# Kernel tuning notes

Hardware: AMD Instinct MI355X
Metric: run time of the kernel (lower is better)

The kernel has to match this reference:

```python
import jax, jax.numpy as jnp
import numpy as np
from jax import lax


def _conv(x, w, b, padding):
    # x: NCHW, w: OIHW
    y = lax.conv_general_dilated(x, w, (1, 1), padding,
                                 dimension_numbers=('NCHW', 'OIHW', 'NCHW'))
    return y + b[None, :, None, None]


def setup_inputs() -> dict:
    key = jax.random.key(0)
    ks = jax.random.split(key, 24)
    B = 64
    d = {
        'p2': jax.random.normal(ks[0], (B, 128, 64, 128), jnp.float32),
        'p3': jax.random.normal(ks[1], (B, 128, 32, 64), jnp.float32),
        'p4': jax.random.normal(ks[2], (B, 128, 16, 32), jnp.float32),
        'p5': jax.random.normal(ks[3], (B, 512, 8, 16), jnp.float32),
    }
    def w(k, shape, fan_in):
        return jax.random.normal(k, shape, jnp.float32) * (1.0 / np.sqrt(fan_in))
    # smooth convs 3x3, 128->128
    for i, name in enumerate(['s1', 's2', 's3']):
        d['w_' + name] = w(ks[4 + 2 * i], (128, 128, 3, 3), 128 * 9)
        d['b_' + name] = jnp.zeros((128,), jnp.float32)
    # tidy convs 1x1
    tidy_cin = [128, 128, 128, 512]
    for i in range(4):
        d['w_t%d' % (i + 1)] = w(ks[10 + i], (1, tidy_cin[i], 1, 1), tidy_cin[i])
        d['b_t%d' % (i + 1)] = jnp.zeros((1,), jnp.float32)
    # pl convs (kH,1) on single channel
    pl_kh = [64, 32, 16, 8]
    for i in range(4):
        d['w_pl%d' % (i + 1)] = w(ks[14 + i], (1, 1, pl_kh[i], 1), pl_kh[i])
        d['b_pl%d' % (i + 1)] = jnp.zeros((1,), jnp.float32)
    return d


def reference(p2, p3, p4, p5,
              w_s1, b_s1, w_s2, b_s2, w_s3, b_s3,
              w_t1, b_t1, w_t2, b_t2, w_t3, b_t3, w_t4, b_t4,
              w_pl1, b_pl1, w_pl2, b_pl2, w_pl3, b_pl3, w_pl4, b_pl4):
    B = p2.shape[0]
    # smooth + relu (p5 has no smooth in the original module)
    q2 = jax.nn.relu(_conv(p2, w_s1, b_s1, 'SAME'))
    q3 = jax.nn.relu(_conv(p3, w_s2, b_s2, 'SAME'))
    q4 = jax.nn.relu(_conv(p4, w_s3, b_s3, 'SAME'))
    # tidy 1x1 -> single score channel
    t1 = _conv(q2, w_t1, b_t1, 'VALID')
    t2 = _conv(q3, w_t2, b_t2, 'VALID')
    t3 = _conv(q4, w_t3, b_t3, 'VALID')
    t4 = _conv(p5, w_t4, b_t4, 'VALID')
    # column-pooling convs collapse height to 1 -> per-column scores
    c1 = _conv(t1, w_pl1, b_pl1, 'VALID').reshape(B, -1)  # [B,128]
    c2 = _conv(t2, w_pl2, b_pl2, 'VALID').reshape(B, -1)  # [B,64]
    c3 = _conv(t3, w_pl3, b_pl3, 'VALID').reshape(B, -1)  # [B,32]
    c4 = _conv(t4, w_pl4, b_pl4, 'VALID').reshape(B, -1)  # [B,16]
    return jnp.concatenate([c1, c2, c3, c4], axis=1)      # [B,240]
```

## Files before the change

### kernel.cpp

```cpp
#include <hip/hip_runtime.h>


typedef short s8v __attribute__((ext_vector_type(8)));
typedef float f4v __attribute__((ext_vector_type(4)));

__device__ __forceinline__ unsigned short f32_bf16_rne(float f) {
  union { float f; unsigned int u; } v;
  v.f = f;
  unsigned int u = v.u;
  u += 0x7FFFu + ((u >> 16) & 1u);
  return (unsigned short)(u >> 16);
}

__global__ void prep_w_k(const float* __restrict__ w1,
                         const float* __restrict__ w2,
                         const float* __restrict__ w3,
                         unsigned short* __restrict__ out) {
  int idx = blockIdx.x * 256 + threadIdx.x;
  if (idx >= 442368) return;
  int i    = idx & 7;
  int cout = (idx >> 3) & 127;
  int t    = idx >> 10;
  int qg = t & 3; t >>= 2;
  int kw = t % 3; t /= 3;
  int kh = t % 3; t /= 3;
  int chunk = t & 3; t >>= 2;
  int s = t;
  const float* w = (s == 0) ? w1 : ((s == 1) ? w2 : w3);
  int cin = chunk * 32 + qg * 8 + i;
  out[idx] = f32_bf16_rne(w[((cout * 128 + cin) * 3 + kh) * 3 + kw]);
}

__global__ void init_out_k(float* __restrict__ out,
                           const float* bt1, const float* bt2,
                           const float* bt3, const float* bt4,
                           const float* wpl1, const float* bpl1,
                           const float* wpl2, const float* bpl2,
                           const float* wpl3, const float* bpl3,
                           const float* wpl4, const float* bpl4) {
  int idx = blockIdx.x * 256 + threadIdx.x;
  if (idx >= 64 * 240) return;
  int c = idx % 240;
  const float* wpl; const float* bpl; const float* bt; int H;
  if (c < 128)      { wpl = wpl1; bpl = bpl1; bt = bt1; H = 64; }
  else if (c < 192) { wpl = wpl2; bpl = bpl2; bt = bt2; H = 32; }
  else if (c < 224) { wpl = wpl3; bpl = bpl3; bt = bt3; H = 16; }
  else              { wpl = wpl4; bpl = bpl4; bt = bt4; H = 8;  }
  float s = 0.f;
  for (int h = 0; h < H; ++h) s += wpl[h];
  out[idx] = bt[0] * s + bpl[0];
}

__global__ void level4_k(const float* __restrict__ p5,
                         const float* __restrict__ w_t4,
                         const float* __restrict__ w_pl4,
                         float* __restrict__ out) {
  int b = blockIdx.x;
  int z = blockIdx.y;
  int t = threadIdx.x;
  int w = t & 15, g = t >> 4;
  const float* base = p5 + (size_t)b * 65536 + z * 16384;
  const float* wt = w_t4 + z * 128;
  float acc = 0.f;
  for (int j = g; j < 1024; j += 16) {
    acc += wt[j >> 3] * w_pl4[j & 7] * base[j * 16 + w];
  }
  acc += __shfl_xor(acc, 16);
  acc += __shfl_xor(acc, 32);
  if ((t & 48) == 0) atomicAdd(&out[b * 240 + 224 + w], acc);
}

template<int H, int W, int R, int COLBASE>
__global__ __launch_bounds__(256, 2)
void conv_level_k(const float* __restrict__ p,
                  const unsigned short* __restrict__ wl,
                  const float* __restrict__ b_s,
                  const float* __restrict__ w_t,
                  const float* __restrict__ w_pl,
                  float* __restrict__ out) {
  constexpr int ROWS = R + 2;
  constexpr int WP = W + 2;
  constexpr int HW = H * W;
  constexpr int NIT = 4 * ROWS * WP;
  __shared__ __align__(16) unsigned short Xs[4][ROWS][WP][8];
  __shared__ __align__(16) unsigned short Ws[3][4][128][8];

  const int tid = threadIdx.x;
  const int wave = tid >> 6, lane = tid & 63;
  const int lm = lane & 15, q = lane >> 4;
  const int h0 = blockIdx.x * R;
  const int b  = blockIdx.y;

  int rr[4], ww[4], xbase[4];
#pragma unroll
  for (int nt = 0; nt < 4; ++nt) {
    int n = wave * 64 + nt * 16 + lm;
    rr[nt] = n / W;
    ww[nt] = n % W;
    xbase[nt] = ((q * ROWS + rr[nt]) * WP + ww[nt]) * 16;
  }
  const int woff = (q * 128 + lm) * 16;

  f4v acc[8][4];
#pragma unroll
  for (int mt = 0; mt < 8; ++mt)
#pragma unroll
    for (int nt = 0; nt < 4; ++nt)
      acc[mt][nt] = (f4v){0.f, 0.f, 0.f, 0.f};

  const s8v Z8 = {0, 0, 0, 0, 0, 0, 0, 0};
  const float* pb = p + (size_t)b * 128 * HW;
  const char* XsB = (const char*)&Xs[0][0][0][0];
  const char* WsB = (const char*)&Ws[0][0][0][0];

  s8v wreg[6];
  const unsigned short* wseg = wl + wave * 512 + lane * 8;
  unsigned short* wdst = &Ws[0][0][0][0] + wave * 512 + lane * 8;

#define LOAD_W(chunk, kh) do {                                        \
    const unsigned short* _s = wseg + ((chunk) * 3 + (kh)) * 12288;   \
    _Pragma("unroll")                                                 \
    for (int s = 0; s < 6; ++s) wreg[s] = *(const s8v*)(_s + s * 2048); \
  } while (0)

#define STORE_W() do {                                                \
    _Pragma("unroll")                                                 \
    for (int s = 0; s < 6; ++s) *(s8v*)(wdst + s * 2048) = wreg[s];   \
  } while (0)

  LOAD_W(0, 0);

  for (int chunk = 0; chunk < 4; ++chunk) {
    __syncthreads();
    for (int it = tid; it < NIT; it += 256) {
      int pos = it % WP;
      int rem = it / WP;
      int row = rem % ROWS;
      int qg  = rem / ROWS;
      int h_in = h0 + row - 1;
      int w_g  = pos - 1;
      s8v v = Z8;
      if (h_in >= 0 && h_in < H && w_g >= 0 && w_g < W) {
        const float* src = pb + (size_t)(chunk * 32 + qg * 8) * HW + h_in * W + w_g;
#pragma unroll
        for (int i = 0; i < 8; ++i) v[i] = (short)f32_bf16_rne(src[(size_t)i * HW]);
      }
      *(s8v*)&Xs[qg][row][pos][0] = v;
    }
    STORE_W();
    __syncthreads();

#pragma unroll
    for (int kh = 0; kh < 3; ++kh) {
      int nc = (kh == 2) ? ((chunk < 3) ? chunk + 1 : 3) : chunk;
      int nk = (kh == 2) ? 0 : kh + 1;
      LOAD_W(nc, nk);

      int xk[4];
#pragma unroll
      for (int nt = 0; nt < 4; ++nt) xk[nt] = xbase[nt] + kh * (WP * 16);

#pragma unroll
      for (int kw = 0; kw < 3; ++kw) {
        s8v bf[4];
#pragma unroll
        for (int nt = 0; nt < 4; ++nt)
          bf[nt] = *(const s8v*)(XsB + xk[nt] + kw * 16);
#pragma unroll
        for (int mt = 0; mt < 8; ++mt) {
          s8v af = *(const s8v*)(WsB + kw * 8192 + mt * 256 + woff);
#pragma unroll
          for (int nt = 0; nt < 4; ++nt)
            acc[mt][nt] = __builtin_amdgcn_mfma_f32_16x16x32_bf16(af, bf[nt], acc[mt][nt], 0, 0, 0);
        }
      }
      if (kh < 2) {
        __syncthreads();
        STORE_W();
        __syncthreads();
      }
    }
  }
#undef LOAD_W
#undef STORE_W

#pragma unroll
  for (int nt = 0; nt < 4; ++nt) {
    float s = 0.f;
#pragma unroll
    for (int mt = 0; mt < 8; ++mt) {
#pragma unroll
      for (int rg = 0; rg < 4; ++rg) {
        int cout = mt * 16 + q * 4 + rg;
        float v = fmaxf(acc[mt][nt][rg] + b_s[cout], 0.f);
        s = fmaf(w_t[cout], v, s);
      }
    }
    s *= w_pl[h0 + rr[nt]];
    s += __shfl_xor(s, 16);
    s += __shfl_xor(s, 32);
    if (lane < 16) atomicAdd(&out[b * 240 + COLBASE + ww[nt]], s);
  }
}

extern "C" void kernel_launch(void* const* d_in, const int* in_sizes, int n_in,
                              void* d_out, int out_size, void* d_ws, size_t ws_size,
                              hipStream_t stream) {
  (void)in_sizes; (void)n_in; (void)out_size; (void)ws_size;
  const float* p2   = (const float*)d_in[0];
  const float* p3   = (const float*)d_in[1];
  const float* p4   = (const float*)d_in[2];
  const float* p5   = (const float*)d_in[3];
  const float* w_s1 = (const float*)d_in[4];
  const float* b_s1 = (const float*)d_in[5];
  const float* w_s2 = (const float*)d_in[6];
  const float* b_s2 = (const float*)d_in[7];
  const float* w_s3 = (const float*)d_in[8];
  const float* b_s3 = (const float*)d_in[9];
  const float* w_t1 = (const float*)d_in[10];
  const float* b_t1 = (const float*)d_in[11];
  const float* w_t2 = (const float*)d_in[12];
  const float* b_t2 = (const float*)d_in[13];
  const float* w_t3 = (const float*)d_in[14];
  const float* b_t3 = (const float*)d_in[15];
  const float* w_t4 = (const float*)d_in[16];
  const float* b_t4 = (const float*)d_in[17];
  const float* w_pl1 = (const float*)d_in[18];
  const float* b_pl1 = (const float*)d_in[19];
  const float* w_pl2 = (const float*)d_in[20];
  const float* b_pl2 = (const float*)d_in[21];
  const float* w_pl3 = (const float*)d_in[22];
  const float* b_pl3 = (const float*)d_in[23];
  const float* w_pl4 = (const float*)d_in[24];
  const float* b_pl4 = (const float*)d_in[25];

  unsigned short* wp = (unsigned short*)d_ws;
  float* out = (float*)d_out;

  prep_w_k<<<dim3(1728), dim3(256), 0, stream>>>(w_s1, w_s2, w_s3, wp);
  init_out_k<<<dim3(60), dim3(256), 0, stream>>>(out, b_t1, b_t2, b_t3, b_t4,
                                                 w_pl1, b_pl1, w_pl2, b_pl2,
                                                 w_pl3, b_pl3, w_pl4, b_pl4);
  conv_level_k<64, 128, 2, 0><<<dim3(32, 64), dim3(256), 0, stream>>>(
      p2, wp, b_s1, w_t1, w_pl1, out);
  conv_level_k<32, 64, 4, 128><<<dim3(8, 64), dim3(256), 0, stream>>>(
      p3, wp + 147456, b_s2, w_t2, w_pl2, out);
  conv_level_k<16, 32, 8, 192><<<dim3(2, 64), dim3(256), 0, stream>>>(
      p4, wp + 294912, b_s3, w_t3, w_pl3, out);
  level4_k<<<dim3(64, 4), dim3(256), 0, stream>>>(p5, w_t4, w_pl4, out);
}
```

Before: 680.1 us.

## Restructure conv kernel to one output row per block with double-buffered pipelined loads

```diff
diff --git a/kernel.cpp b/kernel.cpp
--- a/kernel.cpp
+++ b/kernel.cpp
@@ -3,6 +3,8 @@
 
 typedef short s8v __attribute__((ext_vector_type(8)));
 typedef float f4v __attribute__((ext_vector_type(4)));
+
+#define BARRIER() asm volatile("s_waitcnt lgkmcnt(0)\n\ts_barrier" ::: "memory")
 
 __device__ __forceinline__ unsigned short f32_bf16_rne(float f) {
   union { float f; unsigned int u; } v;
@@ -70,136 +72,168 @@
   if ((t & 48) == 0) atomicAdd(&out[b * 240 + 224 + w], acc);
 }
 
-template<int H, int W, int R, int COLBASE>
+template<int H, int W, int COLBASE>
 __global__ __launch_bounds__(256, 2)
-void conv_level_k(const float* __restrict__ p,
+void conv_fused_k(const float* __restrict__ p,
                   const unsigned short* __restrict__ wl,
                   const float* __restrict__ b_s,
                   const float* __restrict__ w_t,
                   const float* __restrict__ w_pl,
                   float* __restrict__ out) {
-  constexpr int ROWS = R + 2;
   constexpr int WP = W + 2;
+  constexpr int NT = (W >= 128) ? 2 : 1;
+  constexpr int AW = W / (16 * NT);
   constexpr int HW = H * W;
-  constexpr int NIT = 4 * ROWS * WP;
-  __shared__ __align__(16) unsigned short Xs[4][ROWS][WP][8];
-  __shared__ __align__(16) unsigned short Ws[3][4][128][8];
+  constexpr int SLOTS = 4 * W;
+  constexpr int SPT = (SLOTS + 255) / 256;
+  __shared__ __align__(16) unsigned short Xs[4][3][WP][8];
+  __shared__ __align__(16) unsigned short Ws[2][3][4][128][8];
 
   const int tid = threadIdx.x;
   const int wave = tid >> 6, lane = tid & 63;
   const int lm = lane & 15, q = lane >> 4;
-  const int h0 = blockIdx.x * R;
+  const int h0 = blockIdx.x;
   const int b  = blockIdx.y;
-
-  int rr[4], ww[4], xbase[4];
-#pragma unroll
-  for (int nt = 0; nt < 4; ++nt) {
-    int n = wave * 64 + nt * 16 + lm;
-    rr[nt] = n / W;
-    ww[nt] = n % W;
-    xbase[nt] = ((q * ROWS + rr[nt]) * WP + ww[nt]) * 16;
-  }
-  const int woff = (q * 128 + lm) * 16;
-
-  f4v acc[8][4];
-#pragma unroll
-  for (int mt = 0; mt < 8; ++mt)
-#pragma unroll
-    for (int nt = 0; nt < 4; ++nt)
-      acc[mt][nt] = (f4v){0.f, 0.f, 0.f, 0.f};
-
-  const s8v Z8 = {0, 0, 0, 0, 0, 0, 0, 0};
   const float* pb = p + (size_t)b * 128 * HW;
-  const char* XsB = (const char*)&Xs[0][0][0][0];
-  const char* WsB = (const char*)&Ws[0][0][0][0];
-
+
+  int sqg[SPT], swp[SPT];
+  bool sok[SPT];
+  const float* sbase[SPT];
+#pragma unroll
+  for (int k = 0; k < SPT; ++k) {
+    int slot = tid + 256 * k;
+    sok[k] = (SLOTS % 256 == 0) ? true : (slot < SLOTS);
+    int qg = slot / W;
+    int wp_ = slot % W;
+    sqg[k] = qg; swp[k] = wp_;
+    sbase[k] = pb + (size_t)(qg * 8) * HW + wp_;
+  }
+  bool rok[3]; int hin[3];
+#pragma unroll
+  for (int r = 0; r < 3; ++r) { hin[r] = h0 + r - 1; rok[r] = (hin[r] >= 0) && (hin[r] < H); }
+
+  float xf[SPT][8];
   s8v wreg[6];
   const unsigned short* wseg = wl + wave * 512 + lane * 8;
-  unsigned short* wdst = &Ws[0][0][0][0] + wave * 512 + lane * 8;
-
-#define LOAD_W(chunk, kh) do {                                        \
-    const unsigned short* _s = wseg + ((chunk) * 3 + (kh)) * 12288;   \
-    _Pragma("unroll")                                                 \
-    for (int s = 0; s < 6; ++s) wreg[s] = *(const s8v*)(_s + s * 2048); \
-  } while (0)
-
-#define STORE_W() do {                                                \
-    _Pragma("unroll")                                                 \
-    for (int s = 0; s < 6; ++s) *(s8v*)(wdst + s * 2048) = wreg[s];   \
-  } while (0)
-
-  LOAD_W(0, 0);
-
-  for (int chunk = 0; chunk < 4; ++chunk) {
-    __syncthreads();
-    for (int it = tid; it < NIT; it += 256) {
-      int pos = it % WP;
-      int rem = it / WP;
-      int row = rem % ROWS;
-      int qg  = rem / ROWS;
-      int h_in = h0 + row - 1;
-      int w_g  = pos - 1;
-      s8v v = Z8;
-      if (h_in >= 0 && h_in < H && w_g >= 0 && w_g < W) {
-        const float* src = pb + (size_t)(chunk * 32 + qg * 8) * HW + h_in * W + w_g;
-#pragma unroll
-        for (int i = 0; i < 8; ++i) v[i] = (short)f32_bf16_rne(src[(size_t)i * HW]);
-      }
-      *(s8v*)&Xs[qg][row][pos][0] = v;
-    }
-    STORE_W();
-    __syncthreads();
-
+  unsigned short* wdstbase = &Ws[0][0][0][0][0] + wave * 512 + lane * 8;
+
+  auto issueW = [&](int t) {
+    const unsigned short* s = wseg + t * 12288;
+#pragma unroll
+    for (int j = 0; j < 6; ++j) wreg[j] = *(const s8v*)(s + j * 2048);
+  };
+  auto writeW = [&](int buf) {
+    unsigned short* d = wdstbase + buf * 12288;
+#pragma unroll
+    for (int j = 0; j < 6; ++j) *(s8v*)(d + j * 2048) = wreg[j];
+  };
+  auto issueXa = [&](float (*arr)[8], int c, int r) {
+#pragma unroll
+    for (int k = 0; k < SPT; ++k) {
+      if (sok[k] && rok[r]) {
+        const float* s = sbase[k] + (size_t)(c * 32) * HW + (size_t)hin[r] * W;
+#pragma unroll
+        for (int i = 0; i < 8; ++i) arr[k][i] = s[(size_t)i * HW];
+      } else {
+#pragma unroll
+        for (int i = 0; i < 8; ++i) arr[k][i] = 0.f;
+      }
+    }
+  };
+  auto writeXa = [&](float (*arr)[8], int r) {
+#pragma unroll
+    for (int k = 0; k < SPT; ++k) {
+      if (sok[k]) {
+        s8v v;
+#pragma unroll
+        for (int i = 0; i < 8; ++i) v[i] = (short)f32_bf16_rne(arr[k][i]);
+        *(s8v*)&Xs[sqg[k]][r][1 + swp[k]][0] = v;
+      }
+    }
+  };
+
+  if (tid < 24) {
+    int qg = tid / 6, r2 = tid % 6;
+    const s8v Z = {0, 0, 0, 0, 0, 0, 0, 0};
+    *(s8v*)&Xs[qg][r2 >> 1][(r2 & 1) ? (WP - 1) : 0][0] = Z;
+  }
+  {
+    float xr0[SPT][8], xr1[SPT][8];
+    issueW(0);
+    issueXa(xr0, 0, 0);
+    issueXa(xr1, 0, 1);
+    issueXa(xf, 0, 2);
+    writeW(0);
+    issueW(1);
+    writeXa(xr0, 0);
+    writeXa(xr1, 1);
+  }
+  BARRIER();
+
+  f4v acc[8][NT];
+#pragma unroll
+  for (int mt = 0; mt < 8; ++mt)
+#pragma unroll
+    for (int t = 0; t < NT; ++t)
+      acc[mt][t] = (f4v){0.f, 0.f, 0.f, 0.f};
+
+  for (int c = 0; c < 4; ++c) {
 #pragma unroll
     for (int kh = 0; kh < 3; ++kh) {
-      int nc = (kh == 2) ? ((chunk < 3) ? chunk + 1 : 3) : chunk;
-      int nk = (kh == 2) ? 0 : kh + 1;
-      LOAD_W(nc, nk);
-
-      int xk[4];
-#pragma unroll
-      for (int nt = 0; nt < 4; ++nt) xk[nt] = xbase[nt] + kh * (WP * 16);
-
-#pragma unroll
-      for (int kw = 0; kw < 3; ++kw) {
-        s8v bf[4];
-#pragma unroll
-        for (int nt = 0; nt < 4; ++nt)
-          bf[nt] = *(const s8v*)(XsB + xk[nt] + kw * 16);
-#pragma unroll
-        for (int mt = 0; mt < 8; ++mt) {
-          s8v af = *(const s8v*)(WsB + kw * 8192 + mt * 256 + woff);
-#pragma unroll
-          for (int nt = 0; nt < 4; ++nt)
-            acc[mt][nt] = __builtin_amdgcn_mfma_f32_16x16x32_bf16(af, bf[nt], acc[mt][nt], 0, 0, 0);
+      const int sidx = c * 3 + kh;
+      if (!(c == 3 && kh == 2)) writeW((sidx + 1) & 1);
+      if (!(c == 3 && kh >= 1)) issueW(sidx + 2);
+      if (kh == 0) {
+        writeXa(xf, 2);
+        if (c < 3) issueXa(xf, c + 1, 0);
+      } else if (kh == 1) {
+        if (c < 3) { writeXa(xf, 0); issueXa(xf, c + 1, 1); }
+      } else {
+        if (c < 3) { writeXa(xf, 1); issueXa(xf, c + 1, 2); }
+      }
+      if (wave < AW) {
+        const unsigned short* WsRd = &Ws[sidx & 1][0][0][0][0];
+#pragma unroll
+        for (int kw = 0; kw < 3; ++kw) {
+          s8v bfv[NT];
+#pragma unroll
+          for (int t = 0; t < NT; ++t) {
+            int n = wave * (16 * NT) + t * 16 + lm;
+            bfv[t] = *(const s8v*)&Xs[q][kh][n + kw][0];
+          }
+#pragma unroll
+          for (int mt = 0; mt < 8; ++mt) {
+            s8v af = *(const s8v*)(WsRd + kw * 4096 + q * 1024 + (mt * 16 + lm) * 8);
+#pragma unroll
+            for (int t = 0; t < NT; ++t)
+              acc[mt][t] = __builtin_amdgcn_mfma_f32_16x16x32_bf16(af, bfv[t], acc[mt][t], 0, 0, 0);
+          }
         }
       }
-      if (kh < 2) {
-        __syncthreads();
-        STORE_W();
-        __syncthreads();
-      }
-    }
-  }
-#undef LOAD_W
-#undef STORE_W
-
-#pragma unroll
-  for (int nt = 0; nt < 4; ++nt) {
-    float s = 0.f;
-#pragma unroll
-    for (int mt = 0; mt < 8; ++mt) {
-#pragma unroll
-      for (int rg = 0; rg < 4; ++rg) {
-        int cout = mt * 16 + q * 4 + rg;
-        float v = fmaxf(acc[mt][nt][rg] + b_s[cout], 0.f);
-        s = fmaf(w_t[cout], v, s);
-      }
-    }
-    s *= w_pl[h0 + rr[nt]];
-    s += __shfl_xor(s, 16);
-    s += __shfl_xor(s, 32);
-    if (lane < 16) atomicAdd(&out[b * 240 + COLBASE + ww[nt]], s);
+      if (!(c == 3 && kh == 2)) BARRIER();
+    }
+  }
+
+  if (wave < AW) {
+    const float wph = w_pl[h0];
+#pragma unroll
+    for (int t = 0; t < NT; ++t) {
+      float s = 0.f;
+#pragma unroll
+      for (int mt = 0; mt < 8; ++mt) {
+#pragma unroll
+        for (int rg = 0; rg < 4; ++rg) {
+          int cout = mt * 16 + q * 4 + rg;
+          float v = fmaxf(acc[mt][t][rg] + b_s[cout], 0.f);
+          s = fmaf(w_t[cout], v, s);
+        }
+      }
+      s *= wph;
+      s += __shfl_xor(s, 16);
+      s += __shfl_xor(s, 32);
+      int n = wave * (16 * NT) + t * 16 + lm;
+      if (lane < 16) atomicAdd(&out[b * 240 + COLBASE + n], s);
+    }
   }
 }
 
@@ -241,11 +275,11 @@
   init_out_k<<<dim3(60), dim3(256), 0, stream>>>(out, b_t1, b_t2, b_t3, b_t4,
                                                  w_pl1, b_pl1, w_pl2, b_pl2,
                                                  w_pl3, b_pl3, w_pl4, b_pl4);
-  conv_level_k<64, 128, 2, 0><<<dim3(32, 64), dim3(256), 0, stream>>>(
+  conv_fused_k<64, 128, 0><<<dim3(64, 64), dim3(256), 0, stream>>>(
       p2, wp, b_s1, w_t1, w_pl1, out);
-  conv_level_k<32, 64, 4, 128><<<dim3(8, 64), dim3(256), 0, stream>>>(
+  conv_fused_k<32, 64, 128><<<dim3(32, 64), dim3(256), 0, stream>>>(
       p3, wp + 147456, b_s2, w_t2, w_pl2, out);
-  conv_level_k<16, 32, 8, 192><<<dim3(2, 64), dim3(256), 0, stream>>>(
+  conv_fused_k<16, 32, 192><<<dim3(16, 64), dim3(256), 0, stream>>>(
       p4, wp + 294912, b_s3, w_t3, w_pl3, out);
   level4_k<<<dim3(64, 4), dim3(256), 0, stream>>>(p5, w_t4, w_pl4, out);
 }
```

Result: faster. 648.4 us (-4.7%).
